# Kernel tuning notes

Measured on AMD Instinct MI355X. Metric: run time of the kernel, lower is better.

Reference implementation:

```python
import jax, jax.numpy as jnp
import numpy as np

EPS = 1e-5

def layer_norm(x, gamma, beta):
    mu = jnp.mean(x, axis=-1, keepdims=True)
    var = jnp.var(x, axis=-1, keepdims=True)
    return (x - mu) * jax.lax.rsqrt(var + EPS) * gamma + beta

def setup_inputs() -> dict:
    key = jax.random.key(0)
    ks = jax.random.split(key, 9)
    B, S, H = 4, 4096, 1024
    x = jax.random.normal(ks[0], (B, S, H), dtype=jnp.float32)
    w1 = jax.random.normal(ks[1], (H, 4 * H), dtype=jnp.float32) * (1.0 / np.sqrt(H))
    b1 = jnp.zeros((4 * H,), dtype=jnp.float32)
    w2 = jax.random.normal(ks[2], (4 * H, H), dtype=jnp.float32) * (1.0 / np.sqrt(4 * H))
    b2 = jnp.zeros((H,), dtype=jnp.float32)
    g1 = jnp.ones((H,), dtype=jnp.float32)
    be1 = jnp.zeros((H,), dtype=jnp.float32)
    g2 = jnp.ones((H,), dtype=jnp.float32)
    be2 = jnp.zeros((H,), dtype=jnp.float32)
    return {"x": x, "w1": w1, "b1": b1, "w2": w2, "b2": b2,
            "g1": g1, "be1": be1, "g2": g2, "be2": be2}

def reference(x, w1, b1, w2, b2, g1, be1, g2, be2):
    # FNet mixing: FFT over hidden dim, then seq dim, take real part
    x_ft = jnp.fft.fft(jnp.fft.fft(x.astype(jnp.float32), axis=-1), axis=-2).real
    h = layer_norm(x + x_ft, g1, be1)
    # FFN with exact GELU (torch nn.GELU default); dropout is identity in eval
    ffn = jax.nn.gelu(h @ w1 + b1, approximate=False) @ w2 + b2
    return layer_norm(h + ffn, g2, be2)
```

## Files before the change

kernel.cpp:

```cpp
#include <hip/hip_runtime.h>
#include <math.h>
#include <stdint.h>

#define DI __device__ __forceinline__
typedef unsigned short u16;
typedef unsigned int   u32;
typedef unsigned long long u64;

typedef __attribute__((ext_vector_type(4))) float f32x4;
typedef __attribute__((ext_vector_type(8))) short bf16x8;

DI float bf2f(u16 v){ return __uint_as_float(((u32)v) << 16); }
DI u16 f2bf(float f){ u32 u = __float_as_uint(f); return (u16)((u + 0x7FFFu + ((u >> 16) & 1u)) >> 16); }
DI u32 pack2(float re, float im){ return (u32)f2bf(re) | ((u32)f2bf(im) << 16); }

DI float gelu_fast(float v){
  float t = v * v;
  float z = v * fmaf(0.0356774081f, t, 0.7978845608f);
  z = fminf(z, 15.0f);
  float e = __expf(2.0f * z);
  return v * e * __frcp_rn(1.0f + e);
}

__global__ __launch_bounds__(256) void transpose_u32(const u32* __restrict__ in, u32* __restrict__ out, int R, int C){
  __shared__ u32 tile[64][65];
  int t = threadIdx.x;
  int c = t & 63, r0 = t >> 6;
  size_t bofs = (size_t)blockIdx.z * (size_t)R * (size_t)C;
  const u32* ib = in  + bofs + (size_t)(blockIdx.y * 64) * C + blockIdx.x * 64;
  u32*       ob = out + bofs + (size_t)(blockIdx.x * 64) * R + blockIdx.y * 64;
  #pragma unroll
  for (int i = 0; i < 16; i++){ int r = r0 + i * 4; tile[r][c] = ib[(size_t)r * C + c]; }
  __syncthreads();
  #pragma unroll
  for (int i = 0; i < 16; i++){ int r = r0 + i * 4; ob[(size_t)r * R + c] = tile[c][r]; }
}

__global__ __launch_bounds__(256) void transpose_w(const float* __restrict__ w1, u16* __restrict__ w1T,
                                                   const float* __restrict__ w2, u16* __restrict__ w2T){
  __shared__ u16 tile[64][65];
  int t = threadIdx.x;
  int c = t & 63, r0 = t >> 6;
  const float* in; u16* out; int R, C, bx, by;
  if (blockIdx.z == 0){ in = w1; out = w1T; R = 1024; C = 4096; bx = blockIdx.x; by = blockIdx.y; }
  else                { in = w2; out = w2T; R = 4096; C = 1024; bx = blockIdx.y; by = blockIdx.x; }
  const float* ib = in  + (size_t)(by * 64) * C + bx * 64;
  u16*         ob = out + (size_t)(bx * 64) * R + by * 64;
  #pragma unroll
  for (int i = 0; i < 16; i++){ int r = r0 + i * 4; tile[r][c] = f2bf(ib[(size_t)r * C + c]); }
  __syncthreads();
  #pragma unroll
  for (int i = 0; i < 16; i++){ int r = r0 + i * 4; ob[(size_t)r * R + c] = tile[c][r]; }
}

template<int LOGN>
DI float2* fft_r4(float2* s, float2* d, int t){
  const int Q = 1 << (LOGN - 2);
  #pragma unroll
  for (int st = 0; st < (LOGN >> 1); ++st){
    const int m = 1 << (2 * st);
    const float ang = -6.28318530717958647692f * (float)m / (float)(1 << LOGN);
    #pragma unroll
    for (int j0 = 0; j0 < Q; j0 += 256){
      int j = j0 + t;
      int p = j >> (2 * st);
      int q = j & (m - 1);
      int o = q + (p << (2 * st + 2));
      float2 a0 = s[j], a1 = s[j + Q], a2 = s[j + 2 * Q], a3 = s[j + 3 * Q];
      float s0r = a0.x + a2.x, s0i = a0.y + a2.y, d0r = a0.x - a2.x, d0i = a0.y - a2.y;
      float s1r = a1.x + a3.x, s1i = a1.y + a3.y, d1r = a1.x - a3.x, d1i = a1.y - a3.y;
      float sn, cs; __sincosf(ang * (float)p, &sn, &cs);
      float t2r = cs * cs - sn * sn, t2i = 2.f * cs * sn;
      float t3r = t2r * cs - t2i * sn, t3i = t2r * sn + t2i * cs;
      float e1r = d0r + d1i, e1i = d0i - d1r;
      float e2r = s0r - s1r, e2i = s0i - s1i;
      float e3r = d0r - d1i, e3i = d0i + d1r;
      d[o]         = make_float2(s0r + s1r, s0i + s1i);
      d[o + m]     = make_float2(cs * e1r - sn * e1i,  cs * e1i + sn * e1r);
      d[o + 2 * m] = make_float2(t2r * e2r - t2i * e2i, t2r * e2i + t2i * e2r);
      d[o + 3 * m] = make_float2(t3r * e3r - t3i * e3i, t3r * e3i + t3i * e3r);
    }
    __syncthreads();
    float2* tp = s; s = d; d = tp;
  }
  return s;
}

__global__ __launch_bounds__(256) void fft_seq(const float* __restrict__ xT, u32* __restrict__ ZT2,
                                               float* __restrict__ Zny){
  __shared__ float2 A[4096], Bb[4096];
  int t = threadIdx.x, g = blockIdx.x;
  const float* r0 = xT + (size_t)(2 * g) * 4096;
  #pragma unroll
  for (int i = 0; i < 4; i++){
    int idx = i * 1024 + t * 4;
    float4 va = *(const float4*)(r0 + idx);
    float4 vb = *(const float4*)(r0 + 4096 + idx);
    A[idx + 0] = make_float2(va.x, vb.x);
    A[idx + 1] = make_float2(va.y, vb.y);
    A[idx + 2] = make_float2(va.z, vb.z);
    A[idx + 3] = make_float2(va.w, vb.w);
  }
  __syncthreads();
  float2* R = fft_r4<12>(A, Bb, t);
  size_t ob0 = (size_t)(2 * g) * 2048;
  #pragma unroll
  for (int i = 0; i < 2; i++){
    int k0 = i * 1024 + t * 4;
    u32 wa[4], wb[4];
    #pragma unroll
    for (int kk = 0; kk < 4; kk++){
      int k = k0 + kk, m = (4096 - k) & 4095;
      float2 zk = R[k], zm = R[m];
      wa[kk] = pack2(0.5f * (zk.x + zm.x), 0.5f * (zk.y - zm.y));
      wb[kk] = pack2(0.5f * (zk.y + zm.y), 0.5f * (zm.x - zk.x));
    }
    *(uint4*)(ZT2 + ob0 + k0)        = make_uint4(wa[0], wa[1], wa[2], wa[3]);
    *(uint4*)(ZT2 + ob0 + 2048 + k0) = make_uint4(wb[0], wb[1], wb[2], wb[3]);
  }
  if (t == 0){ float2 z = R[2048]; Zny[2 * g] = z.x; Zny[2 * g + 1] = z.y; }
}

DI void block_stats4(float a1, float a2, float b1, float b2, int t,
                     float& mA, float& iA, float& mB, float& iB){
  __shared__ float sh[4][4];
  #pragma unroll
  for (int o = 32; o > 0; o >>= 1){
    a1 += __shfl_down(a1, o); a2 += __shfl_down(a2, o);
    b1 += __shfl_down(b1, o); b2 += __shfl_down(b2, o);
  }
  if ((t & 63) == 0){ int w = t >> 6; sh[w][0] = a1; sh[w][1] = a2; sh[w][2] = b1; sh[w][3] = b2; }
  __syncthreads();
  float SA = sh[0][0] + sh[1][0] + sh[2][0] + sh[3][0];
  float QA = sh[0][1] + sh[1][1] + sh[2][1] + sh[3][1];
  float SB = sh[0][2] + sh[1][2] + sh[2][2] + sh[3][2];
  float QB = sh[0][3] + sh[1][3] + sh[2][3] + sh[3][3];
  mA = SA * (1.f / 1024.f); iA = rsqrtf(QA * (1.f / 1024.f) - mA * mA + 1e-5f);
  mB = SB * (1.f / 1024.f); iB = rsqrtf(QB * (1.f / 1024.f) - mB * mB + 1e-5f);
}

__global__ __launch_bounds__(256) void fft_hid_ln(const u32* __restrict__ Z2, const float* __restrict__ Zny,
    const float* __restrict__ x, const float* __restrict__ g1, const float* __restrict__ be1,
    u16* __restrict__ h){
  __shared__ float2 A[1024], Bb[1024];
  int t = threadIdx.x, id = blockIdx.x;
  int b = id / 2049, k = id - b * 2049;
  int idx = t * 4;
  if (k == 2048){
    float4 v = *(const float4*)(Zny + b * 1024 + idx);
    A[idx + 0] = make_float2(v.x, 0.f); A[idx + 1] = make_float2(v.y, 0.f);
    A[idx + 2] = make_float2(v.z, 0.f); A[idx + 3] = make_float2(v.w, 0.f);
  } else {
    uint4 zv = *(const uint4*)(Z2 + ((size_t)b * 2048 + k) * 1024 + idx);
    A[idx + 0] = make_float2(bf2f((u16)(zv.x & 0xffffu)), bf2f((u16)(zv.x >> 16)));
    A[idx + 1] = make_float2(bf2f((u16)(zv.y & 0xffffu)), bf2f((u16)(zv.y >> 16)));
    A[idx + 2] = make_float2(bf2f((u16)(zv.z & 0xffffu)), bf2f((u16)(zv.z >> 16)));
    A[idx + 3] = make_float2(bf2f((u16)(zv.w & 0xffffu)), bf2f((u16)(zv.w >> 16)));
  }
  __syncthreads();
  float2* R = fft_r4<10>(A, Bb, t);
  int rowA = b * 4096 + k;
  bool two = (k >= 1) && (k <= 2047);
  int rowB = b * 4096 + (4096 - k);
  float4 xa = *(const float4*)(x + (size_t)rowA * 1024 + idx);
  float vA0 = R[idx + 0].x + xa.x, vA1 = R[idx + 1].x + xa.y;
  float vA2 = R[idx + 2].x + xa.z, vA3 = R[idx + 3].x + xa.w;
  float vB0 = 0.f, vB1 = 0.f, vB2 = 0.f, vB3 = 0.f;
  if (two){
    float4 xb = *(const float4*)(x + (size_t)rowB * 1024 + idx);
    vB0 = R[(1024 - (idx + 0)) & 1023].x + xb.x;
    vB1 = R[(1024 - (idx + 1)) & 1023].x + xb.y;
    vB2 = R[(1024 - (idx + 2)) & 1023].x + xb.z;
    vB3 = R[(1024 - (idx + 3)) & 1023].x + xb.w;
  }
  float mA, iA, mB, iB;
  block_stats4(vA0 + vA1 + vA2 + vA3, vA0 * vA0 + vA1 * vA1 + vA2 * vA2 + vA3 * vA3,
               vB0 + vB1 + vB2 + vB3, vB0 * vB0 + vB1 * vB1 + vB2 * vB2 + vB3 * vB3,
               t, mA, iA, mB, iB);
  float4 gv = *(const float4*)(g1 + idx);
  float4 bv = *(const float4*)(be1 + idx);
  ushort4 oA;
  oA.x = f2bf((vA0 - mA) * iA * gv.x + bv.x);
  oA.y = f2bf((vA1 - mA) * iA * gv.y + bv.y);
  oA.z = f2bf((vA2 - mA) * iA * gv.z + bv.z);
  oA.w = f2bf((vA3 - mA) * iA * gv.w + bv.w);
  *(ushort4*)(h + (size_t)rowA * 1024 + idx) = oA;
  if (two){
    ushort4 oB;
    oB.x = f2bf((vB0 - mB) * iB * gv.x + bv.x);
    oB.y = f2bf((vB1 - mB) * iB * gv.y + bv.y);
    oB.z = f2bf((vB2 - mB) * iB * gv.z + bv.z);
    oB.w = f2bf((vB3 - mB) * iB * gv.w + bv.w);
    *(ushort4*)(h + (size_t)rowB * 1024 + idx) = oB;
  }
}

__global__ __launch_bounds__(256) void ln_rows(const u16* __restrict__ yv, const float* __restrict__ g,
    const float* __restrict__ be, float* __restrict__ o){
  int t = threadIdx.x;
  size_t base = (size_t)blockIdx.x * 1024;
  int idx = t * 4;
  ushort4 v4 = *(const ushort4*)(yv + base + idx);
  float v0 = bf2f(v4.x), v1 = bf2f(v4.y), v2 = bf2f(v4.z), v3 = bf2f(v4.w);
  float mA, iA, mB, iB;
  block_stats4(v0 + v1 + v2 + v3, v0 * v0 + v1 * v1 + v2 * v2 + v3 * v3, 0.f, 0.f, t, mA, iA, mB, iB);
  float4 gv = *(const float4*)(g + idx);
  float4 bv = *(const float4*)(be + idx);
  float4 ov;
  ov.x = (v0 - mA) * iA * gv.x + bv.x;
  ov.y = (v1 - mA) * iA * gv.y + bv.y;
  ov.z = (v2 - mA) * iA * gv.z + bv.z;
  ov.w = (v3 - mA) * iA * gv.w + bv.w;
  *(float4*)(o + base + idx) = ov;
}

typedef const __attribute__((address_space(1))) void* as1cp;
typedef __attribute__((address_space(3))) void* as3p;
DI void async_copy16(const void* g, void* l){
  __builtin_amdgcn_global_load_lds((as1cp)(u64)g, (as3p)(u32)(u64)l, 16, 0, 0);
}
DI void bar(){
  asm volatile("" ::: "memory");
  __builtin_amdgcn_s_barrier();
  asm volatile("" ::: "memory");
}

template<int DOGELU>
__global__ __launch_bounds__(512, 2) void gemm256(const u16* __restrict__ A, const u16* __restrict__ Bm,
    const float* __restrict__ bias, const u16* __restrict__ resid, u16* __restrict__ C,
    int M, int N, int K, int gn_shift, int npg_shift, int mpg, int bpg, int npt)
{
  __shared__ u16 sA[2][2][8192];
  __shared__ u16 sB[2][2][8192];
  int t = threadIdx.x, wv = t >> 6, ln = t & 63;

  int bid = blockIdx.x;
  int c8 = bid & 7, j0 = bid >> 3;
  int ng = c8 & ((1 << gn_shift) - 1);
  int mg = c8 >> gn_shift;
  int npg_m1 = (1 << npg_shift) - 1;

  int wm = wv >> 2, wn = wv & 3;
  int lt = ln & 15;
  int cs = (((ln >> 4) ^ ((ln >> 1) & 3)) << 3);
  int arow = (wm * 128 + lt) * 32 + cs;
  int brow = (wn * 64 + lt) * 32 + cs;
  int srow = wv * 32 + (ln >> 2);
  int gch  = ((ln & 3) ^ ((srow >> 1) & 3)) << 3;
  int ldof = wv * 1024 + ln * 8;
  int NT = K >> 6;

  #define STAGE(g0, g1, kc, unit) do{ \
    async_copy16((g0) + (kc), (unit) + ldof); \
    async_copy16((g1) + (kc), (unit) + 512 + ldof); }while(0)
  #define PROLOGUE() do{ \
    STAGE(gA0, gA1, 0,  &sA[0][0][0]); \
    STAGE(gB0, gB1, 0,  &sB[0][0][0]); \
    STAGE(gA0, gA1, 32, &sA[0][1][0]); \
    STAGE(gB0, gB1, 32, &sB[0][1][0]); \
    STAGE(gA0, gA1, 64, &sA[1][0][0]); \
    STAGE(gB0, gB1, 64, &sB[1][0][0]); \
    STAGE(gA0, gA1, 96, &sA[1][1][0]); }while(0)

  int jt = j0;
  int n0 = (((ng << npg_shift) + (jt & npg_m1)) << 8);
  int m0 = ((mg * mpg + (jt >> npg_shift)) << 8);
  const u16* gA0 = A  + (size_t)(m0 + srow) * K + gch;
  const u16* gA1 = gA0 + (size_t)16 * K;
  const u16* gB0 = Bm + (size_t)(n0 + srow) * K + gch;
  const u16* gB1 = gB0 + (size_t)16 * K;
  PROLOGUE();
  asm volatile("s_waitcnt vmcnt(6)" ::: "memory");
  bar();

  for (int s = 0; s < npt; ++s){
    f32x4 acc[8][4];
    #pragma unroll
    for (int mf = 0; mf < 8; mf++)
      #pragma unroll
      for (int nf = 0; nf < 4; nf++) acc[mf][nf] = (f32x4){0.f, 0.f, 0.f, 0.f};

    for (int kt = 0; kt < NT; ++kt){
      int buf = kt & 1;
      u16* a0s = &sA[buf][0][0];
      u16* a1s = &sA[buf][1][0];
      u16* b0s = &sB[buf][0][0];
      u16* b1s = &sB[buf][1][0];
      u16* bn1 = &sB[buf ^ 1][1][0];
      bool st1 = (kt + 1) < NT;
      bool st2 = (kt + 2) < NT;
      int kb1 = (kt + 1) << 6, kb2 = (kt + 2) << 6;
      bf16x8 af1[8], af2[8], b1r[4], b2r[4];

      #pragma unroll
      for (int mf = 0; mf < 8; mf++) af1[mf] = *(const bf16x8*)(a0s + arow + mf * 512);
      #pragma unroll
      for (int nf = 0; nf < 4; nf++) b1r[nf] = *(const bf16x8*)(b0s + brow + nf * 512);
      if (st1) STAGE(gB0, gB1, kb1 + 32, bn1);
      bar();
      __builtin_amdgcn_s_setprio(1);
      #pragma unroll
      for (int mf = 0; mf < 8; mf++){
        acc[mf][0] = __builtin_amdgcn_mfma_f32_16x16x32_bf16(af1[mf], b1r[0], acc[mf][0], 0, 0, 0);
        acc[mf][1] = __builtin_amdgcn_mfma_f32_16x16x32_bf16(af1[mf], b1r[1], acc[mf][1], 0, 0, 0);
      }
      __builtin_amdgcn_s_setprio(0);
      bar();

      #pragma unroll
      for (int mf = 0; mf < 8; mf++) af2[mf] = *(const bf16x8*)(a1s + arow + mf * 512);
      #pragma unroll
      for (int nf = 0; nf < 4; nf++) b2r[nf] = *(const bf16x8*)(b1s + brow + nf * 512);
      if (st2) STAGE(gA0, gA1, kb2, a0s);
      bar();
      __builtin_amdgcn_s_setprio(1);
      #pragma unroll
      for (int mf = 0; mf < 8; mf++){
        acc[mf][2] = __builtin_amdgcn_mfma_f32_16x16x32_bf16(af1[mf], b1r[2], acc[mf][2], 0, 0, 0);
        acc[mf][3] = __builtin_amdgcn_mfma_f32_16x16x32_bf16(af1[mf], b1r[3], acc[mf][3], 0, 0, 0);
      }
      __builtin_amdgcn_s_setprio(0);
      asm volatile("s_waitcnt lgkmcnt(0)" ::: "memory");
      bar();

      if (st2) STAGE(gB0, gB1, kb2, b0s);
      bar();
      __builtin_amdgcn_s_setprio(1);
      #pragma unroll
      for (int mf = 0; mf < 8; mf++){
        acc[mf][0] = __builtin_amdgcn_mfma_f32_16x16x32_bf16(af2[mf], b2r[0], acc[mf][0], 0, 0, 0);
        acc[mf][1] = __builtin_amdgcn_mfma_f32_16x16x32_bf16(af2[mf], b2r[1], acc[mf][1], 0, 0, 0);
      }
      __builtin_amdgcn_s_setprio(0);
      bar();

      if (st2) STAGE(gA0, gA1, kb2 + 32, a1s);
      bar();
      __builtin_amdgcn_s_setprio(1);
      #pragma unroll
      for (int mf = 0; mf < 8; mf++){
        acc[mf][2] = __builtin_amdgcn_mfma_f32_16x16x32_bf16(af2[mf], b2r[2], acc[mf][2], 0, 0, 0);
        acc[mf][3] = __builtin_amdgcn_mfma_f32_16x16x32_bf16(af2[mf], b2r[3], acc[mf][3], 0, 0, 0);
      }
      __builtin_amdgcn_s_setprio(0);
      if (st2) asm volatile("s_waitcnt vmcnt(6)" ::: "memory");
      else     asm volatile("s_waitcnt vmcnt(0)" ::: "memory");
      bar();
    }

    int em0 = m0, en0 = n0;
    if (s + 1 < npt){
      jt = j0 + (s + 1) * bpg;
      n0 = (((ng << npg_shift) + (jt & npg_m1)) << 8);
      m0 = ((mg * mpg + (jt >> npg_shift)) << 8);
      gA0 = A  + (size_t)(m0 + srow) * K + gch;
      gA1 = gA0 + (size_t)16 * K;
      gB0 = Bm + (size_t)(n0 + srow) * K + gch;
      gB1 = gB0 + (size_t)16 * K;
      PROLOGUE();
    }

    int colq = lt, rq = ln >> 4;
    #pragma unroll
    for (int mf = 0; mf < 8; mf++){
      int mr = em0 + wm * 128 + mf * 16 + rq * 4;
      #pragma unroll
      for (int nf = 0; nf < 4; nf++){
        int col = en0 + wn * 64 + nf * 16 + colq;
        float bv = bias[col];
        #pragma unroll
        for (int i = 0; i < 4; i++){
          float v = acc[mf][nf][i] + bv;
          if (DOGELU){
            v = gelu_fast(v);
          } else {
            v += bf2f(resid[(size_t)(mr + i) * N + col]);
          }
          C[(size_t)(mr + i) * N + col] = f2bf(v);
        }
      }
    }

    if (s + 1 < npt){
      asm volatile("s_waitcnt vmcnt(6)" ::: "memory");
      bar();
    }
  }
  #undef PROLOGUE
  #undef STAGE
}

static inline int ilog2(int v){ int s = 0; while ((1 << s) < v) ++s; return s; }

extern "C" void kernel_launch(void* const* d_in, const int* in_sizes, int n_in,
                              void* d_out, int out_size, void* d_ws, size_t ws_size,
                              hipStream_t stream){
  const float* x   = (const float*)d_in[0];
  const float* w1  = (const float*)d_in[1];
  const float* b1  = (const float*)d_in[2];
  const float* w2  = (const float*)d_in[3];
  const float* b2  = (const float*)d_in[4];
  const float* g1  = (const float*)d_in[5];
  const float* be1 = (const float*)d_in[6];
  const float* g2  = (const float*)d_in[7];
  const float* be2 = (const float*)d_in[8];
  float* out = (float*)d_out;
  char* ws = (char*)d_ws;
  const size_t MB = (size_t)1 << 20;
  float* xT  = (float*)(ws);
  u32*  ZT2  = (u32*)(ws + 64 * MB);
  float* Zny = (float*)(ws + 96 * MB);
  u32*  Z2   = (u32*)(ws);
  u16*  h    = (u16*)(ws + 32 * MB);
  u16*  w1T  = (u16*)(ws + 64 * MB);
  u16*  w2T  = (u16*)(ws + 72 * MB);
  u16*  u    = (u16*)(ws + 80 * MB);
  u16*  y    = (u16*)(ws);
  dim3 blk(256, 1, 1);
  dim3 blk2(512, 1, 1);

  transpose_u32<<<dim3(16, 64, 4), blk, 0, stream>>>((const u32*)x, (u32*)xT, 4096, 1024);
  fft_seq      <<<dim3(2048, 1, 1), blk, 0, stream>>>(xT, ZT2, Zny);
  transpose_u32<<<dim3(32, 16, 4), blk, 0, stream>>>(ZT2, Z2, 1024, 2048);
  fft_hid_ln   <<<dim3(4 * 2049, 1, 1), blk, 0, stream>>>(Z2, Zny, x, g1, be1, h);

  transpose_w<<<dim3(64, 16, 2), blk, 0, stream>>>(w1, w1T, w2, w2T);
  int nch = (ws_size >= (size_t)209 * MB) ? 1 : (ws_size >= (size_t)145 * MB) ? 2 : 4;
  int Mc = 16384 / nch;
  for (int ch = 0; ch < nch; ++ch){
    const u16* hch = h + (size_t)ch * Mc * 1024;
    u16* ych = y + (size_t)ch * Mc * 1024;
    {
      int tm = Mc >> 8, tn = 16, gn = 2;
      int tiles = tm * tn;
      int grid = tiles < 256 ? tiles : 256;
      int npt = tiles / grid, bpg = grid >> 3;
      int npgs = ilog2(tn >> gn);
      int mpg = tm >> (3 - gn);
      gemm256<1><<<dim3(grid), blk2, 0, stream>>>(hch, w1T, b1, (const u16*)nullptr, u,
                                                  Mc, 4096, 1024, gn, npgs, mpg, bpg, npt);
    }
    {
      int tm = Mc >> 8, tn = 4, gn = 0;
      int tiles = tm * tn;
      int grid = tiles < 256 ? tiles : 256;
      int npt = tiles / grid, bpg = grid >> 3;
      int npgs = ilog2(tn >> gn);
      int mpg = tm >> (3 - gn);
      gemm256<0><<<dim3(grid), blk2, 0, stream>>>(u, w2T, b2, hch, ych,
                                                  Mc, 1024, 4096, gn, npgs, mpg, bpg, npt);
    }
  }
  ln_rows<<<dim3(16384, 1, 1), blk, 0, stream>>>(y, g2, be2, out);
}
```

Before: 549.3 us.

## Software-pipeline LDS fragment reads across k-iterations in GEMM main loop

Restructures the GEMM k-loop so the register fragments for the next k-slice are read from LDS while MFMAs on the current slice run, using two persistent register sets (E/F) instead of per-iteration loads followed by immediate use. This is meant to hide LDS read latency behind matrix-core work and removes an explicit lgkmcnt(0) wait. It increases register pressure (extra 24 bf16x8 fragments live), which may reduce occupancy or cause spills, and changes the vmcnt wait conditions, which affects correctness of the async-copy ordering.

```diff
diff --git a/kernel.cpp b/kernel.cpp
--- a/kernel.cpp
+++ b/kernel.cpp
@@ -261,6 +261,17 @@
     STAGE(gA0, gA1, 64, &sA[1][0][0]); \
     STAGE(gB0, gB1, 64, &sB[1][0][0]); \
     STAGE(gA0, gA1, 96, &sA[1][1][0]); }while(0)
+  #define RDSET(dstA, dstB, asrc, bsrc) do{ \
+    _Pragma("unroll") \
+    for (int mf = 0; mf < 8; mf++) dstA[mf] = *(const bf16x8*)((asrc) + arow + mf * 512); \
+    _Pragma("unroll") \
+    for (int nf = 0; nf < 4; nf++) dstB[nf] = *(const bf16x8*)((bsrc) + brow + nf * 512); }while(0)
+  #define MMH(aS, bS, n0_, n1_) do{ \
+    _Pragma("unroll") \
+    for (int mf = 0; mf < 8; mf++){ \
+      acc[mf][n0_] = __builtin_amdgcn_mfma_f32_16x16x32_bf16(aS[mf], bS[n0_], acc[mf][n0_], 0, 0, 0); \
+      acc[mf][n1_] = __builtin_amdgcn_mfma_f32_16x16x32_bf16(aS[mf], bS[n1_], acc[mf][n1_], 0, 0, 0); \
+    } }while(0)
 
   int jt = j0;
   int n0 = (((ng << npg_shift) + (jt & npg_m1)) << 8);
@@ -273,6 +284,8 @@
   asm volatile("s_waitcnt vmcnt(6)" ::: "memory");
   bar();
 
+  bf16x8 aE[8], bE[4], aF[8], bF[4];
+
   for (int s = 0; s < npt; ++s){
     f32x4 acc[8][4];
     #pragma unroll
@@ -280,70 +293,53 @@
       #pragma unroll
       for (int nf = 0; nf < 4; nf++) acc[mf][nf] = (f32x4){0.f, 0.f, 0.f, 0.f};
 
+    RDSET(aE, bE, &sA[0][0][0], &sB[0][0][0]);
+
     for (int kt = 0; kt < NT; ++kt){
       int buf = kt & 1;
       u16* a0s = &sA[buf][0][0];
       u16* a1s = &sA[buf][1][0];
       u16* b0s = &sB[buf][0][0];
       u16* b1s = &sB[buf][1][0];
+      u16* an  = &sA[buf ^ 1][0][0];
+      u16* bn  = &sB[buf ^ 1][0][0];
       u16* bn1 = &sB[buf ^ 1][1][0];
       bool st1 = (kt + 1) < NT;
       bool st2 = (kt + 2) < NT;
       int kb1 = (kt + 1) << 6, kb2 = (kt + 2) << 6;
-      bf16x8 af1[8], af2[8], b1r[4], b2r[4];
-
-      #pragma unroll
-      for (int mf = 0; mf < 8; mf++) af1[mf] = *(const bf16x8*)(a0s + arow + mf * 512);
-      #pragma unroll
-      for (int nf = 0; nf < 4; nf++) b1r[nf] = *(const bf16x8*)(b0s + brow + nf * 512);
+
+      RDSET(aF, bF, a1s, b1s);
       if (st1) STAGE(gB0, gB1, kb1 + 32, bn1);
       bar();
       __builtin_amdgcn_s_setprio(1);
-      #pragma unroll
-      for (int mf = 0; mf < 8; mf++){
-        acc[mf][0] = __builtin_amdgcn_mfma_f32_16x16x32_bf16(af1[mf], b1r[0], acc[mf][0], 0, 0, 0);
-        acc[mf][1] = __builtin_amdgcn_mfma_f32_16x16x32_bf16(af1[mf], b1r[1], acc[mf][1], 0, 0, 0);
+      MMH(aE, bE, 0, 1);
+      __builtin_amdgcn_s_setprio(0);
+      bar();
+
+      if (st2) STAGE(gA0, gA1, kb2, a0s);
+      bar();
+      __builtin_amdgcn_s_setprio(1);
+      MMH(aE, bE, 2, 3);
+      __builtin_amdgcn_s_setprio(0);
+      bar();
+
+      if (st1){
+        asm volatile("s_waitcnt vmcnt(6)" ::: "memory");
+        RDSET(aE, bE, an, bn);
       }
+      if (st2) STAGE(gB0, gB1, kb2, b0s);
+      bar();
+      __builtin_amdgcn_s_setprio(1);
+      MMH(aF, bF, 0, 1);
       __builtin_amdgcn_s_setprio(0);
       bar();
 
-      #pragma unroll
-      for (int mf = 0; mf < 8; mf++) af2[mf] = *(const bf16x8*)(a1s + arow + mf * 512);
-      #pragma unroll
-      for (int nf = 0; nf < 4; nf++) b2r[nf] = *(const bf16x8*)(b1s + brow + nf * 512);
-      if (st2) STAGE(gA0, gA1, kb2, a0s);
+      if (st2) STAGE(gA0, gA1, kb2 + 32, a1s);
       bar();
       __builtin_amdgcn_s_setprio(1);
-      #pragma unroll
-      for (int mf = 0; mf < 8; mf++){
-        acc[mf][2] = __builtin_amdgcn_mfma_f32_16x16x32_bf16(af1[mf], b1r[2], acc[mf][2], 0, 0, 0);
-        acc[mf][3] = __builtin_amdgcn_mfma_f32_16x16x32_bf16(af1[mf], b1r[3], acc[mf][3], 0, 0, 0);
-      }
+      MMH(aF, bF, 2, 3);
       __builtin_amdgcn_s_setprio(0);
-      asm volatile("s_waitcnt lgkmcnt(0)" ::: "memory");
-      bar();
-
-      if (st2) STAGE(gB0, gB1, kb2, b0s);
-      bar();
-      __builtin_amdgcn_s_setprio(1);
-      #pragma unroll
-      for (int mf = 0; mf < 8; mf++){
-        acc[mf][0] = __builtin_amdgcn_mfma_f32_16x16x32_bf16(af2[mf], b2r[0], acc[mf][0], 0, 0, 0);
-        acc[mf][1] = __builtin_amdgcn_mfma_f32_16x16x32_bf16(af2[mf], b2r[1], acc[mf][1], 0, 0, 0);
-      }
-      __builtin_amdgcn_s_setprio(0);
-      bar();
-
-      if (st2) STAGE(gA0, gA1, kb2 + 32, a1s);
-      bar();
-      __builtin_amdgcn_s_setprio(1);
-      #pragma unroll
-      for (int mf = 0; mf < 8; mf++){
-        acc[mf][2] = __builtin_amdgcn_mfma_f32_16x16x32_bf16(af2[mf], b2r[2], acc[mf][2], 0, 0, 0);
-        acc[mf][3] = __builtin_amdgcn_mfma_f32_16x16x32_bf16(af2[mf], b2r[3], acc[mf][3], 0, 0, 0);
-      }
-      __builtin_amdgcn_s_setprio(0);
-      if (st2) asm volatile("s_waitcnt vmcnt(6)" ::: "memory");
+      if (st1) asm volatile("s_waitcnt vmcnt(6)" ::: "memory");
       else     asm volatile("s_waitcnt vmcnt(0)" ::: "memory");
       bar();
     }
@@ -386,6 +382,8 @@
       bar();
     }
   }
+  #undef MMH
+  #undef RDSET
   #undef PROLOGUE
   #undef STAGE
 }
```

Measured after the change: 538.4 us. 1.02x faster.
